# Optimization experiments

Hardware: AMD Instinct MI355X
Metric: run time of the kernel (lower is better)

Reference implementation:

```python
import jax, jax.numpy as jnp
import numpy as np

B, T = 32, 256
INPUT_DIM, TRAJ_TYPE_DIM = 10000, 32
HIDDEN, N_LAYERS, EMBED = 512, 2, 256
OUTPUT_DIM = 10000


def setup_inputs() -> dict:
    key = jax.random.key(0)
    ks = jax.random.split(key, 16)
    s = 0.05
    inp = {
        "locations": jax.random.randint(ks[0], (B, T), 0, INPUT_DIM),
        "times": jax.random.uniform(ks[1], (B, T, 1), dtype=jnp.float32),
        "labels": jax.random.randint(ks[2], (B,), 0, TRAJ_TYPE_DIM),
        "emb_table": jax.random.normal(ks[3], (INPUT_DIM, EMBED), jnp.float32) * s,
        "traj_emb": jax.random.normal(ks[4], (TRAJ_TYPE_DIM, HIDDEN * N_LAYERS), jnp.float32) * s,
        "w_ih0": jax.random.normal(ks[5], (3 * HIDDEN, EMBED + 1), jnp.float32) * s,
        "w_hh0": jax.random.normal(ks[6], (3 * HIDDEN, HIDDEN), jnp.float32) * s,
        "b_ih0": jax.random.normal(ks[7], (3 * HIDDEN,), jnp.float32) * s,
        "b_hh0": jax.random.normal(ks[8], (3 * HIDDEN,), jnp.float32) * s,
        "w_ih1": jax.random.normal(ks[9], (3 * HIDDEN, HIDDEN), jnp.float32) * s,
        "w_hh1": jax.random.normal(ks[10], (3 * HIDDEN, HIDDEN), jnp.float32) * s,
        "b_ih1": jax.random.normal(ks[11], (3 * HIDDEN,), jnp.float32) * s,
        "b_hh1": jax.random.normal(ks[12], (3 * HIDDEN,), jnp.float32) * s,
        "fc_w": jax.random.normal(ks[13], (OUTPUT_DIM + 1, HIDDEN), jnp.float32) * s,
        "fc_b": jax.random.normal(ks[14], (OUTPUT_DIM + 1,), jnp.float32) * s,
    }
    return inp


def _gru_layer(x_tbf, h0, w_ih, w_hh, b_ih, b_hh):
    # x_tbf: [T, B, F]; h0: [B, H]. Standard torch GRU cell math.
    x_gates = jnp.einsum("tbf,gf->tbg", x_tbf, w_ih) + b_ih  # [T,B,3H]

    def step(h, xg):
        hg = h @ w_hh.T + b_hh
        xr, xz, xn = jnp.split(xg, 3, axis=-1)
        hr, hz, hn = jnp.split(hg, 3, axis=-1)
        r = jax.nn.sigmoid(xr + hr)
        z = jax.nn.sigmoid(xz + hz)
        n = jnp.tanh(xn + r * hn)
        h_new = (1.0 - z) * n + z * h
        return h_new, h_new

    _, outs = jax.lax.scan(step, h0, x_gates)
    return outs  # [T, B, H]


def reference(locations, times, labels, emb_table, traj_emb,
              w_ih0, w_hh0, b_ih0, b_hh0, w_ih1, w_hh1, b_ih1, b_hh1,
              fc_w, fc_b):
    # init hidden: [B, L*H] -> flat view -> [L, B, H] (matches torch .view)
    h0 = traj_emb[labels].reshape(N_LAYERS, -1, HIDDEN)
    x = jnp.concatenate([emb_table[locations], times], axis=-1)  # [B,T,E+1]
    x = jnp.swapaxes(x, 0, 1)  # [T,B,E+1]
    x = _gru_layer(x, h0[0], w_ih0, w_hh0, b_ih0, b_hh0)
    x = _gru_layer(x, h0[1], w_ih1, w_hh1, b_ih1, b_hh1)
    out = jnp.swapaxes(x, 0, 1)  # [B,T,H]
    out = jax.nn.relu(out) @ fc_w.T + fc_b  # [B,T,OUT+1]
    location = jax.nn.log_softmax(out[:, :, :-1], axis=-1)
    time = jax.nn.sigmoid(out[:, :, -1])
    return (location, time)
```

## Files before the change

### kernel.cpp

```cpp
#include <hip/hip_runtime.h>

typedef unsigned short u16;
typedef __bf16 bf16x8 __attribute__((ext_vector_type(8)));
typedef float f32x4 __attribute__((ext_vector_type(4)));

#define DEVI __device__ __forceinline__

DEVI u16 f2b(float f) {
  union { float f; unsigned u; } c; c.f = f;
  unsigned r = c.u + 0x7FFFu + ((c.u >> 16) & 1u);
  return (u16)(r >> 16);
}

DEVI float sigm(float x) { return 1.f / (1.f + __expf(-x)); }
DEVI float tanhfast(float x) {
  x = fminf(fmaxf(x, -15.f), 15.f);
  float e = __expf(2.f * x);
  return (e - 1.f) / (e + 1.f);
}

DEVI void async16(const void* g, void* l) {
  __builtin_amdgcn_global_load_lds((const __attribute__((address_space(1))) void*)g,
                                   (__attribute__((address_space(3))) void*)l, 16, 0, 0);
}

DEVI f32x4 ld16cc(const u16* p) {
  f32x4 r;
  asm volatile("global_load_dwordx4 %0, %1, off sc0 sc1" : "=v"(r) : "v"(p) : "memory");
  return r;
}

__global__ __launch_bounds__(256) void k_castpad(const float* __restrict__ src, u16* __restrict__ dst,
                                                 int srows, int scols, int drows, int dcols) {
  size_t n = (size_t)drows * dcols;
  for (size_t i = blockIdx.x * 256 + threadIdx.x; i < n; i += (size_t)gridDim.x * 256) {
    int r = (int)(i / dcols), c = (int)(i % dcols);
    float v = (r < srows && c < scols) ? src[(size_t)r * scols + c] : 0.f;
    dst[i] = f2b(v);
  }
}

__global__ __launch_bounds__(256) void k_embed(const int* __restrict__ loc, const float* __restrict__ times,
                                               const float* __restrict__ emb, u16* __restrict__ x0) {
  int m = blockIdx.x * 4 + (threadIdx.x >> 6);
  int s = threadIdx.x & 63;
  int b = m & 31, t = m >> 5;
  int li = loc[b * 256 + t];
  const float4* er = (const float4*)(emb + (size_t)li * 256);
  u16* xr = x0 + (size_t)m * 288;
  float4 v = er[s];
  ushort4 u;
  u.x = f2b(v.x); u.y = f2b(v.y); u.z = f2b(v.z); u.w = f2b(v.w);
  *(ushort4*)(xr + s * 4) = u;
  if (s == 0) xr[256] = f2b(times[b * 256 + t]);
  else if (s <= 31) xr[256 + s] = 0;
}

__global__ __launch_bounds__(256) void k_hinit(const float* __restrict__ traj, const int* __restrict__ labels,
                                               u16* __restrict__ dst, int layer) {
  int idx = blockIdx.x * 256 + threadIdx.x;
  if (idx < 16384) {
    int fidx = layer * 16384 + idx;
    dst[idx] = f2b(traj[(size_t)labels[fidx >> 10] * 1024 + (fidx & 1023)]);
  }
}

template <int MODE>
__global__ __launch_bounds__(256) void k_gemm(const u16* __restrict__ A, const u16* __restrict__ Bw,
                                              const float* __restrict__ bias, float* __restrict__ C,
                                              int N, int K, float* __restrict__ tptr) {
  __shared__ __align__(16) u16 As[128 * 32];
  __shared__ __align__(16) u16 Bs[128 * 32];
  const int tid = threadIdx.x;
  const int lane = tid & 63, wid = tid >> 6;
  const int tn = blockIdx.x, tm = blockIdx.y;
  const int wm = wid >> 1, wn = wid & 1;

  f32x4 acc[4][4] = {};

  const int r0 = tid >> 2;
  const int cb0 = (tid * 16) & 63;

  for (int k0 = 0; k0 < K; k0 += 32) {
    __syncthreads();
#pragma unroll
    for (int p = 0; p < 2; ++p) {
      int row = r0 + p * 64;
      const u16* ga = A + (size_t)(tm * 128 + row) * K + k0 + (cb0 >> 1);
      async16(ga, (void*)(As + wid * 512 + p * 2048));
      const u16* gb = Bw + (size_t)(tn * 128 + row) * K + k0 + (cb0 >> 1);
      async16(gb, (void*)(Bs + wid * 512 + p * 2048));
    }
    asm volatile("s_waitcnt vmcnt(0)" ::: "memory");
    __syncthreads();
    bf16x8 af[4], bf[4];
#pragma unroll
    for (int i = 0; i < 4; ++i) {
      af[i] = *reinterpret_cast<const bf16x8*>(As + (wm * 64 + i * 16 + (lane & 15)) * 32 + ((lane >> 4) * 8));
      bf[i] = *reinterpret_cast<const bf16x8*>(Bs + (wn * 64 + i * 16 + (lane & 15)) * 32 + ((lane >> 4) * 8));
    }
#pragma unroll
    for (int i = 0; i < 4; ++i)
#pragma unroll
      for (int j = 0; j < 4; ++j)
        acc[i][j] = __builtin_amdgcn_mfma_f32_16x16x32_bf16(af[i], bf[j], acc[i][j], 0, 0, 0);
  }

  const int row0 = tm * 128 + wm * 64;
  const int col0 = tn * 128 + wn * 64;
#pragma unroll
  for (int i = 0; i < 4; ++i)
#pragma unroll
    for (int j = 0; j < 4; ++j)
#pragma unroll
      for (int r = 0; r < 4; ++r) {
        int row = row0 + i * 16 + ((lane >> 4) * 4) + r;
        int col = col0 + j * 16 + (lane & 15);
        float v = acc[i][j][r];
        if (MODE == 0) {
          C[(size_t)row * N + col] = v + bias[col];
        } else {
          int orow = ((row & 31) << 8) + (row >> 5);
          if (col < 10000) C[(size_t)orow * 10000 + col] = v + bias[col];
          else if (col == 10000) tptr[orow] = sigm(v + bias[col]);
        }
      }
}

#define NB 64

__global__ __launch_bounds__(512, 2) void k_scan2(
    const float* __restrict__ xg0,
    const u16* __restrict__ whh0, const float* __restrict__ bhh0,
    const u16* __restrict__ wih1, const float* __restrict__ bih1,
    const u16* __restrict__ whh1, const float* __restrict__ bhh1,
    const float* __restrict__ traj, const int* __restrict__ labels,
    u16* __restrict__ h0x, u16* __restrict__ h1x, float* __restrict__ x1x,
    u16* __restrict__ h1seq, int* __restrict__ flags)
{
  const int tid = threadIdx.x, bid = blockIdx.x;
  const int role = bid >> 5, blk = bid & 31;
  const int lane = tid & 63, wid = tid >> 6;
  __shared__ float smD[2][3][16][16];

  const int eb = tid >> 4, ejj = tid & 15;
  const int jg = (blk << 4) + ejj;

  const float* bhh = (role == 0) ? bhh0 : bhh1;
  int fidx = (role == 1 ? 16384 : 0) + eb * 512 + jg;
  float h_own = traj[(size_t)labels[fidx >> 10] * 1024 + (fidx & 1023)];
  const float bh_r = bhh[jg], bh_z = bhh[512 + jg], bh_n = bhh[1024 + jg];

  const int mt = (wid < 6) ? wid / 3 : 0, nt = (wid < 6) ? wid % 3 : 0;
  bf16x8 bfragH[16];
  bf16x8 bfragX[16];
  float bX = 0.f;
  if (wid < 6) {
    const u16* wh = (role == 0) ? whh0 : whh1;
    const u16* wrow = wh + (size_t)(nt * 512 + (blk << 4) + (lane & 15)) * 512 + ((lane >> 4) * 8);
#pragma unroll
    for (int ks = 0; ks < 16; ++ks)
      bfragH[ks] = *reinterpret_cast<const bf16x8*>(wrow + ks * 32);
    if (role == 0) {
      const u16* xrow = wih1 + (size_t)(nt * 512 + (blk << 4) + (lane & 15)) * 512 + ((lane >> 4) * 8);
#pragma unroll
      for (int ks = 0; ks < 16; ++ks)
        bfragX[ks] = *reinterpret_cast<const bf16x8*>(xrow + ks * 32);
      bX = bih1[nt * 512 + (blk << 4) + (lane & 15)];
    }
  }

  const u16* hsrc = (role == 0) ? h0x : h1x;
  u16* hdst = (role == 0) ? h0x : h1x;

  for (int s = 0; s < 258; ++s) {
    const int wp = s & 1, rp = (s + 1) & 1;
    if (role == 0) {
      if (s <= 256) {
        float gxr = 0.f, gxz = 0.f, gxn = 0.f;
        if (s < 256) {
          const float* q = xg0 + (size_t)s * 49152 + eb * 1536 + jg;
          gxr = q[0]; gxz = q[512]; gxn = q[1024];
        }
        if (wid < 6) {
          const u16* hs = hsrc + (rp << 14) + ((mt * 16 + (lane & 15)) << 9) + ((lane >> 4) * 8);
          f32x4 afr[16];
#pragma unroll
          for (int ks = 0; ks < 16; ++ks) afr[ks] = ld16cc(hs + ks * 32);
          asm volatile("s_waitcnt vmcnt(0)" ::: "memory");
          __builtin_amdgcn_sched_barrier(0);
          const int col = lane & 15, rb = (lane >> 4) << 2;
          if (s < 256) {
            f32x4 a0 = {0.f, 0.f, 0.f, 0.f}, a1 = {0.f, 0.f, 0.f, 0.f};
#pragma unroll
            for (int ks = 0; ks < 8; ++ks) {
              a0 = __builtin_amdgcn_mfma_f32_16x16x32_bf16(__builtin_bit_cast(bf16x8, afr[2 * ks]),     bfragH[2 * ks],     a0, 0, 0, 0);
              a1 = __builtin_amdgcn_mfma_f32_16x16x32_bf16(__builtin_bit_cast(bf16x8, afr[2 * ks + 1]), bfragH[2 * ks + 1], a1, 0, 0, 0);
            }
#pragma unroll
            for (int r = 0; r < 4; ++r) smD[mt][nt][rb + r][col] = a0[r] + a1[r];
          }
          if (s >= 1) {
            f32x4 c0 = {0.f, 0.f, 0.f, 0.f}, c1 = {0.f, 0.f, 0.f, 0.f};
#pragma unroll
            for (int ks = 0; ks < 8; ++ks) {
              c0 = __builtin_amdgcn_mfma_f32_16x16x32_bf16(__builtin_bit_cast(bf16x8, afr[2 * ks]),     bfragX[2 * ks],     c0, 0, 0, 0);
              c1 = __builtin_amdgcn_mfma_f32_16x16x32_bf16(__builtin_bit_cast(bf16x8, afr[2 * ks + 1]), bfragX[2 * ks + 1], c1, 0, 0, 0);
            }
            float* xp = x1x + wp * 49152;
#pragma unroll
            for (int r = 0; r < 4; ++r) {
              int ebr = mt * 16 + rb + r;
              __hip_atomic_store(xp + ((ebr * 3 + nt) << 9) + (blk << 4) + col,
                                 c0[r] + c1[r] + bX, __ATOMIC_RELAXED, __HIP_MEMORY_SCOPE_AGENT);
            }
          }
        }
        if (s < 256) {
          __syncthreads();
          float Dr = smD[eb >> 4][0][eb & 15][ejj] + bh_r;
          float Dz = smD[eb >> 4][1][eb & 15][ejj] + bh_z;
          float Dn = smD[eb >> 4][2][eb & 15][ejj] + bh_n;
          float r = sigm(gxr + Dr);
          float z = sigm(gxz + Dz);
          float n = tanhfast(gxn + r * Dn);
          h_own = (1.f - z) * n + z * h_own;
          unsigned hv = f2b(h_own);
          unsigned oth = __shfl_xor(hv, 1);
          if (!(ejj & 1))
            __hip_atomic_store((unsigned*)(hdst + (wp << 14)) + (((eb << 9) + jg) >> 1),
                               hv | (oth << 16), __ATOMIC_RELAXED, __HIP_MEMORY_SCOPE_AGENT);
        }
      }
    } else {
      if (s >= 2) {
        float* xp = x1x + rp * 49152 + ((eb * 3) << 9) + jg;
        float gxr = __hip_atomic_load(xp,        __ATOMIC_RELAXED, __HIP_MEMORY_SCOPE_AGENT);
        float gxz = __hip_atomic_load(xp + 512,  __ATOMIC_RELAXED, __HIP_MEMORY_SCOPE_AGENT);
        float gxn = __hip_atomic_load(xp + 1024, __ATOMIC_RELAXED, __HIP_MEMORY_SCOPE_AGENT);
        if (wid < 6) {
          const u16* hs = hsrc + (rp << 14) + ((mt * 16 + (lane & 15)) << 9) + ((lane >> 4) * 8);
          f32x4 afr[16];
#pragma unroll
          for (int ks = 0; ks < 16; ++ks) afr[ks] = ld16cc(hs + ks * 32);
          asm volatile("s_waitcnt vmcnt(0)" ::: "memory");
          __builtin_amdgcn_sched_barrier(0);
          f32x4 a0 = {0.f, 0.f, 0.f, 0.f}, a1 = {0.f, 0.f, 0.f, 0.f};
#pragma unroll
          for (int ks = 0; ks < 8; ++ks) {
            a0 = __builtin_amdgcn_mfma_f32_16x16x32_bf16(__builtin_bit_cast(bf16x8, afr[2 * ks]),     bfragH[2 * ks],     a0, 0, 0, 0);
            a1 = __builtin_amdgcn_mfma_f32_16x16x32_bf16(__builtin_bit_cast(bf16x8, afr[2 * ks + 1]), bfragH[2 * ks + 1], a1, 0, 0, 0);
          }
          const int col = lane & 15, rb = (lane >> 4) << 2;
#pragma unroll
          for (int r = 0; r < 4; ++r) smD[mt][nt][rb + r][col] = a0[r] + a1[r];
        }
        __syncthreads();
        float Dr = smD[eb >> 4][0][eb & 15][ejj] + bh_r;
        float Dz = smD[eb >> 4][1][eb & 15][ejj] + bh_z;
        float Dn = smD[eb >> 4][2][eb & 15][ejj] + bh_n;
        float r = sigm(gxr + Dr);
        float z = sigm(gxz + Dz);
        float n = tanhfast(gxn + r * Dn);
        h_own = (1.f - z) * n + z * h_own;
        unsigned hv = f2b(h_own);
        unsigned oth = __shfl_xor(hv, 1);
        if (!(ejj & 1))
          __hip_atomic_store((unsigned*)(hdst + (wp << 14)) + (((eb << 9) + jg) >> 1),
                             hv | (oth << 16), __ATOMIC_RELAXED, __HIP_MEMORY_SCOPE_AGENT);
        h1seq[((size_t)((s - 2) * 32 + eb) << 9) + jg] = f2b(fmaxf(h_own, 0.f));
      }
    }
    if (s < 257) {
      asm volatile("s_waitcnt vmcnt(0)" ::: "memory");
      __syncthreads();
      if (tid == 0) {
        __hip_atomic_fetch_add(flags + ((s * 8 + (bid & 7)) << 4), 1,
                               __ATOMIC_RELAXED, __HIP_MEMORY_SCOPE_AGENT);
        int* fb = flags + ((s * 8) << 4);
        int sum;
        do {
          sum = 0;
#pragma unroll
          for (int i = 0; i < 8; ++i)
            sum += __hip_atomic_load(fb + (i << 4), __ATOMIC_RELAXED, __HIP_MEMORY_SCOPE_AGENT);
        } while (sum < NB);
      }
      __syncthreads();
    }
  }
}

__global__ __launch_bounds__(256) void k_logsoftmax(float* __restrict__ out) {
  const int row = blockIdx.x, tid = threadIdx.x;
  float* p = out + (size_t)row * 10000;
  const int n_own = (tid < 16) ? 40 : 39;
  float v[40];
  float mx = -3.4e38f;
#pragma unroll
  for (int i = 0; i < 40; ++i)
    if (i < n_own) { v[i] = p[i * 256 + tid]; mx = fmaxf(mx, v[i]); }
  for (int o = 32; o; o >>= 1) mx = fmaxf(mx, __shfl_xor(mx, o));
  __shared__ float sm[4], ss[4];
  if ((tid & 63) == 0) sm[tid >> 6] = mx;
  __syncthreads();
  mx = fmaxf(fmaxf(sm[0], sm[1]), fmaxf(sm[2], sm[3]));
  float s = 0.f;
#pragma unroll
  for (int i = 0; i < 40; ++i)
    if (i < n_own) s += __expf(v[i] - mx);
  for (int o = 32; o; o >>= 1) s += __shfl_xor(s, o);
  if ((tid & 63) == 0) ss[tid >> 6] = s;
  __syncthreads();
  s = ss[0] + ss[1] + ss[2] + ss[3];
  float lse = mx + __logf(s);
#pragma unroll
  for (int i = 0; i < 40; ++i)
    if (i < n_own) p[i * 256 + tid] = v[i] - lse;
}

extern "C" void kernel_launch(void* const* d_in, const int* in_sizes, int n_in,
                              void* d_out, int out_size, void* d_ws, size_t ws_size,
                              hipStream_t stream) {
  (void)in_sizes; (void)n_in; (void)out_size;
  const int*   loc    = (const int*)  d_in[0];
  const float* times  = (const float*)d_in[1];
  const int*   labels = (const int*)  d_in[2];
  const float* emb    = (const float*)d_in[3];
  const float* traj   = (const float*)d_in[4];
  const float* w_ih0  = (const float*)d_in[5];
  const float* w_hh0  = (const float*)d_in[6];
  const float* b_ih0  = (const float*)d_in[7];
  const float* b_hh0  = (const float*)d_in[8];
  const float* w_ih1  = (const float*)d_in[9];
  const float* w_hh1  = (const float*)d_in[10];
  const float* b_ih1  = (const float*)d_in[11];
  const float* b_hh1  = (const float*)d_in[12];
  const float* fc_w   = (const float*)d_in[13];
  const float* fc_b   = (const float*)d_in[14];

  if (ws_size < 29800000) return;

  char* ws = (char*)d_ws;
  size_t off = 0;
  auto alloc = [&](size_t b) { size_t r = off; off += (b + 255) & ~(size_t)255; return r; };
  int*   flags = (int*)  (ws + alloc(258 * 8 * 16 * 4));
  u16*   h0x   = (u16*)  (ws + alloc(2 * 32 * 512 * 2));
  u16*   h1x   = (u16*)  (ws + alloc(2 * 32 * 512 * 2));
  float* x1x   = (float*)(ws + alloc(2 * 32 * 3 * 512 * 4));
  u16*   x0    = (u16*)  (ws + alloc((size_t)8192 * 288 * 2));
  u16*   wih0b = (u16*)  (ws + alloc((size_t)1536 * 288 * 2));
  u16*   whh0b = (u16*)  (ws + alloc((size_t)1536 * 512 * 2));
  u16*   wih1b = (u16*)  (ws + alloc((size_t)1536 * 512 * 2));
  u16*   whh1b = (u16*)  (ws + alloc((size_t)1536 * 512 * 2));
  u16*   fcwb  = (u16*)  (ws + alloc((size_t)10112 * 512 * 2));
  u16*   h1seq = (u16*)  (ws + alloc((size_t)8192 * 512 * 2));

  float* outp = (float*)d_out;
  float* xg0  = outp;
  float* tptr = outp + 81920000;

  hipMemsetAsync(flags, 0, 258 * 8 * 16 * 4, stream);
  k_castpad<<<1024, 256, 0, stream>>>(w_ih0, wih0b, 1536, 257, 1536, 288);
  k_castpad<<<1024, 256, 0, stream>>>(w_hh0, whh0b, 1536, 512, 1536, 512);
  k_castpad<<<1024, 256, 0, stream>>>(w_ih1, wih1b, 1536, 512, 1536, 512);
  k_castpad<<<1024, 256, 0, stream>>>(w_hh1, whh1b, 1536, 512, 1536, 512);
  k_castpad<<<1024, 256, 0, stream>>>(fc_w, fcwb, 10001, 512, 10112, 512);
  k_embed<<<2048, 256, 0, stream>>>(loc, times, emb, x0);
  k_gemm<0><<<dim3(12, 64), 256, 0, stream>>>(x0, wih0b, b_ih0, xg0, 1536, 288, nullptr);
  k_hinit<<<64, 256, 0, stream>>>(traj, labels, h0x + 16384, 0);
  k_hinit<<<64, 256, 0, stream>>>(traj, labels, h1x + 16384, 1);
  k_scan2<<<NB, 512, 0, stream>>>(xg0, whh0b, b_hh0, wih1b, b_ih1, whh1b, b_hh1,
                                  traj, labels, h0x, h1x, x1x, h1seq, flags);
  k_gemm<1><<<dim3(79, 64), 256, 0, stream>>>(h1seq, fcwb, fc_b, outp, 10112, 512, tptr);
  k_logsoftmax<<<8192, 256, 0, stream>>>(outp);
}
```

Before: 1.841 ms.

## Replace global grid barrier in GRU scan with per-step dataflow tags

The persistent two-layer GRU scan no longer uses a global all-block barrier every timestep. Each block now publishes a per-step tag (replicated 4x to spread polling) and waits only on the tags it depends on, so layer 0 can run up to several steps ahead of layer 1 through an 8-deep x1x ring buffer. The W_ih1 fragments move from registers into swizzled LDS to relieve register pressure. The risks are extra polling traffic, LDS reads on the critical path, and subtle ordering correctness under relaxed atomics.

Measured after the change: 1.735 ms. 1.06x faster.

```diff
diff --git a/kernel.cpp b/kernel.cpp
--- a/kernel.cpp
+++ b/kernel.cpp
@@ -65,6 +65,11 @@
   }
 }
 
+__global__ __launch_bounds__(128) void k_taginit(unsigned* __restrict__ tag0) {
+  int t = threadIdx.x;
+  tag0[(t >> 5) * 259 * 32 + (t & 31)] = 1u;
+}
+
 template <int MODE>
 __global__ __launch_bounds__(256) void k_gemm(const u16* __restrict__ A, const u16* __restrict__ Bw,
                                               const float* __restrict__ bias, float* __restrict__ C,
@@ -127,21 +132,21 @@
       }
 }
 
-#define NB 64
-
-__global__ __launch_bounds__(512, 2) void k_scan2(
-    const float* __restrict__ xg0,
-    const u16* __restrict__ whh0, const float* __restrict__ bhh0,
-    const u16* __restrict__ wih1, const float* __restrict__ bih1,
-    const u16* __restrict__ whh1, const float* __restrict__ bhh1,
-    const float* __restrict__ traj, const int* __restrict__ labels,
-    u16* __restrict__ h0x, u16* __restrict__ h1x, float* __restrict__ x1x,
-    u16* __restrict__ h1seq, int* __restrict__ flags)
+__global__ __launch_bounds__(512) __attribute__((amdgpu_waves_per_eu(2, 2)))
+void k_scan3(const float* __restrict__ xg0,
+             const u16* __restrict__ whh0, const float* __restrict__ bhh0,
+             const u16* __restrict__ wih1, const float* __restrict__ bih1,
+             const u16* __restrict__ whh1, const float* __restrict__ bhh1,
+             const float* __restrict__ traj, const int* __restrict__ labels,
+             u16* __restrict__ h0x, u16* __restrict__ h1x, float* __restrict__ x1x,
+             u16* __restrict__ h1seq, unsigned* __restrict__ tag0, unsigned* __restrict__ tag1)
 {
   const int tid = threadIdx.x, bid = blockIdx.x;
   const int role = bid >> 5, blk = bid & 31;
   const int lane = tid & 63, wid = tid >> 6;
+  const int rep = bid & 3;
   __shared__ float smD[2][3][16][16];
+  __shared__ __align__(16) u16 xlds[24576];
 
   const int eb = tid >> 4, ejj = tid & 15;
   const int jg = (blk << 4) + ejj;
@@ -153,7 +158,6 @@
 
   const int mt = (wid < 6) ? wid / 3 : 0, nt = (wid < 6) ? wid % 3 : 0;
   bf16x8 bfragH[16];
-  bf16x8 bfragX[16];
   float bX = 0.f;
   if (wid < 6) {
     const u16* wh = (role == 0) ? whh0 : whh1;
@@ -161,80 +165,103 @@
 #pragma unroll
     for (int ks = 0; ks < 16; ++ks)
       bfragH[ks] = *reinterpret_cast<const bf16x8*>(wrow + ks * 32);
-    if (role == 0) {
-      const u16* xrow = wih1 + (size_t)(nt * 512 + (blk << 4) + (lane & 15)) * 512 + ((lane >> 4) * 8);
-#pragma unroll
-      for (int ks = 0; ks < 16; ++ks)
-        bfragX[ks] = *reinterpret_cast<const bf16x8*>(xrow + ks * 32);
-      bX = bih1[nt * 512 + (blk << 4) + (lane & 15)];
-    }
-  }
+    if (role == 0) bX = bih1[nt * 512 + (blk << 4) + (lane & 15)];
+  }
+  if (role == 0) {
+    for (int c = tid; c < 3072; c += 512) {
+      int row = c >> 6, o16 = c & 63;
+      int grow = (row >> 4) * 512 + (blk << 4) + (row & 15);
+      const float4* src = (const float4*)(wih1 + (size_t)grow * 512 + o16 * 8);
+      int byte = (row << 10) + ((o16 * 16) ^ ((row & 7) << 4));
+      *(float4*)((char*)xlds + byte) = *src;
+    }
+  }
+  __syncthreads();
 
   const u16* hsrc = (role == 0) ? h0x : h1x;
   u16* hdst = (role == 0) ? h0x : h1x;
+  unsigned* mytag = (role == 0) ? tag0 : tag1;
 
   for (int s = 0; s < 258; ++s) {
-    const int wp = s & 1, rp = (s + 1) & 1;
+    if (role == 0 && s == 257) break;
+    const int rp = (s + 1) & 1, wp = s & 1;
+
     if (role == 0) {
-      if (s <= 256) {
-        float gxr = 0.f, gxz = 0.f, gxn = 0.f;
+      float gxr = 0.f, gxz = 0.f, gxn = 0.f;
+      if (s < 256) {
+        const float* q = xg0 + (size_t)s * 49152 + eb * 1536 + jg;
+        gxr = q[0]; gxz = q[512]; gxn = q[1024];
+      }
+      {
+        const unsigned* tp;
+        if (lane < 32)       tp = tag0 + ((size_t)(rep * 259 + s)) * 32 + lane;
+        else if (s >= 9)     tp = tag1 + ((size_t)(rep * 259 + (s - 6))) * 32 + (lane - 32);
+        else                 tp = tag0 + ((size_t)(rep * 259 + s)) * 32 + (lane - 32);
+        while (__ballot(__hip_atomic_load(tp, __ATOMIC_RELAXED, __HIP_MEMORY_SCOPE_AGENT) != 0u) != ~0ull) {}
+      }
+      if (wid < 6) {
+        const u16* hs = hsrc + (rp << 14) + ((mt * 16 + (lane & 15)) << 9) + ((lane >> 4) * 8);
+        f32x4 afr[16];
+#pragma unroll
+        for (int ks = 0; ks < 16; ++ks) afr[ks] = ld16cc(hs + ks * 32);
+        asm volatile("s_waitcnt vmcnt(0)" ::: "memory");
+        __builtin_amdgcn_sched_barrier(0);
+        const int col = lane & 15, rb = (lane >> 4) << 2;
         if (s < 256) {
-          const float* q = xg0 + (size_t)s * 49152 + eb * 1536 + jg;
-          gxr = q[0]; gxz = q[512]; gxn = q[1024];
-        }
-        if (wid < 6) {
-          const u16* hs = hsrc + (rp << 14) + ((mt * 16 + (lane & 15)) << 9) + ((lane >> 4) * 8);
-          f32x4 afr[16];
-#pragma unroll
-          for (int ks = 0; ks < 16; ++ks) afr[ks] = ld16cc(hs + ks * 32);
-          asm volatile("s_waitcnt vmcnt(0)" ::: "memory");
-          __builtin_amdgcn_sched_barrier(0);
-          const int col = lane & 15, rb = (lane >> 4) << 2;
-          if (s < 256) {
-            f32x4 a0 = {0.f, 0.f, 0.f, 0.f}, a1 = {0.f, 0.f, 0.f, 0.f};
-#pragma unroll
-            for (int ks = 0; ks < 8; ++ks) {
-              a0 = __builtin_amdgcn_mfma_f32_16x16x32_bf16(__builtin_bit_cast(bf16x8, afr[2 * ks]),     bfragH[2 * ks],     a0, 0, 0, 0);
-              a1 = __builtin_amdgcn_mfma_f32_16x16x32_bf16(__builtin_bit_cast(bf16x8, afr[2 * ks + 1]), bfragH[2 * ks + 1], a1, 0, 0, 0);
-            }
-#pragma unroll
-            for (int r = 0; r < 4; ++r) smD[mt][nt][rb + r][col] = a0[r] + a1[r];
+          f32x4 a0 = {0.f, 0.f, 0.f, 0.f}, a1 = {0.f, 0.f, 0.f, 0.f};
+#pragma unroll
+          for (int ks = 0; ks < 8; ++ks) {
+            a0 = __builtin_amdgcn_mfma_f32_16x16x32_bf16(__builtin_bit_cast(bf16x8, afr[2 * ks]),     bfragH[2 * ks],     a0, 0, 0, 0);
+            a1 = __builtin_amdgcn_mfma_f32_16x16x32_bf16(__builtin_bit_cast(bf16x8, afr[2 * ks + 1]), bfragH[2 * ks + 1], a1, 0, 0, 0);
           }
-          if (s >= 1) {
-            f32x4 c0 = {0.f, 0.f, 0.f, 0.f}, c1 = {0.f, 0.f, 0.f, 0.f};
-#pragma unroll
-            for (int ks = 0; ks < 8; ++ks) {
-              c0 = __builtin_amdgcn_mfma_f32_16x16x32_bf16(__builtin_bit_cast(bf16x8, afr[2 * ks]),     bfragX[2 * ks],     c0, 0, 0, 0);
-              c1 = __builtin_amdgcn_mfma_f32_16x16x32_bf16(__builtin_bit_cast(bf16x8, afr[2 * ks + 1]), bfragX[2 * ks + 1], c1, 0, 0, 0);
-            }
-            float* xp = x1x + wp * 49152;
-#pragma unroll
-            for (int r = 0; r < 4; ++r) {
-              int ebr = mt * 16 + rb + r;
-              __hip_atomic_store(xp + ((ebr * 3 + nt) << 9) + (blk << 4) + col,
-                                 c0[r] + c1[r] + bX, __ATOMIC_RELAXED, __HIP_MEMORY_SCOPE_AGENT);
-            }
+#pragma unroll
+          for (int r = 0; r < 4; ++r) smD[mt][nt][rb + r][col] = a0[r] + a1[r];
+        }
+        if (s >= 1) {
+          const char* xbase = (const char*)xlds + ((nt * 16 + col) << 10);
+          const int cb = (lane >> 4) << 4;
+          const int swz = ((col & 7) << 4);
+          f32x4 c0 = {0.f, 0.f, 0.f, 0.f}, c1 = {0.f, 0.f, 0.f, 0.f};
+#pragma unroll
+          for (int ks = 0; ks < 8; ++ks) {
+            bf16x8 x0 = *(const bf16x8*)(xbase + (((2 * ks) * 64 + cb) ^ swz));
+            bf16x8 x1 = *(const bf16x8*)(xbase + (((2 * ks + 1) * 64 + cb) ^ swz));
+            c0 = __builtin_amdgcn_mfma_f32_16x16x32_bf16(__builtin_bit_cast(bf16x8, afr[2 * ks]),     x0, c0, 0, 0, 0);
+            c1 = __builtin_amdgcn_mfma_f32_16x16x32_bf16(__builtin_bit_cast(bf16x8, afr[2 * ks + 1]), x1, c1, 0, 0, 0);
           }
-        }
-        if (s < 256) {
-          __syncthreads();
-          float Dr = smD[eb >> 4][0][eb & 15][ejj] + bh_r;
-          float Dz = smD[eb >> 4][1][eb & 15][ejj] + bh_z;
-          float Dn = smD[eb >> 4][2][eb & 15][ejj] + bh_n;
-          float r = sigm(gxr + Dr);
-          float z = sigm(gxz + Dz);
-          float n = tanhfast(gxn + r * Dn);
-          h_own = (1.f - z) * n + z * h_own;
-          unsigned hv = f2b(h_own);
-          unsigned oth = __shfl_xor(hv, 1);
-          if (!(ejj & 1))
-            __hip_atomic_store((unsigned*)(hdst + (wp << 14)) + (((eb << 9) + jg) >> 1),
-                               hv | (oth << 16), __ATOMIC_RELAXED, __HIP_MEMORY_SCOPE_AGENT);
-        }
+          float* xp = x1x + (size_t)((s - 1) & 7) * 49152;
+#pragma unroll
+          for (int r = 0; r < 4; ++r) {
+            int ebr = mt * 16 + rb + r;
+            __hip_atomic_store(xp + ((ebr * 3 + nt) << 9) + (blk << 4) + col,
+                               c0[r] + c1[r] + bX, __ATOMIC_RELAXED, __HIP_MEMORY_SCOPE_AGENT);
+          }
+        }
+      }
+      __syncthreads();
+      if (s < 256) {
+        float Dr = smD[eb >> 4][0][eb & 15][ejj] + bh_r;
+        float Dz = smD[eb >> 4][1][eb & 15][ejj] + bh_z;
+        float Dn = smD[eb >> 4][2][eb & 15][ejj] + bh_n;
+        float r = sigm(gxr + Dr);
+        float z = sigm(gxz + Dz);
+        float n = tanhfast(gxn + r * Dn);
+        h_own = (1.f - z) * n + z * h_own;
+        unsigned hv = f2b(h_own);
+        unsigned oth = __shfl_xor(hv, 1);
+        if (!(ejj & 1))
+          __hip_atomic_store((unsigned*)(hdst + (wp << 14)) + (((eb << 9) + jg) >> 1),
+                             hv | (oth << 16), __ATOMIC_RELAXED, __HIP_MEMORY_SCOPE_AGENT);
       }
     } else {
       if (s >= 2) {
-        float* xp = x1x + rp * 49152 + ((eb * 3) << 9) + jg;
+        {
+          const unsigned* tp = (lane < 32)
+              ? tag0 + ((size_t)(rep * 259 + s)) * 32 + lane
+              : tag1 + ((size_t)(rep * 259 + s)) * 32 + (lane - 32);
+          while (__ballot(__hip_atomic_load(tp, __ATOMIC_RELAXED, __HIP_MEMORY_SCOPE_AGENT) != 0u) != ~0ull) {}
+        }
+        float* xp = x1x + (size_t)((s - 2) & 7) * 49152 + ((eb * 3) << 9) + jg;
         float gxr = __hip_atomic_load(xp,        __ATOMIC_RELAXED, __HIP_MEMORY_SCOPE_AGENT);
         float gxz = __hip_atomic_load(xp + 512,  __ATOMIC_RELAXED, __HIP_MEMORY_SCOPE_AGENT);
         float gxn = __hip_atomic_load(xp + 1024, __ATOMIC_RELAXED, __HIP_MEMORY_SCOPE_AGENT);
@@ -271,22 +298,13 @@
         h1seq[((size_t)((s - 2) * 32 + eb) << 9) + jg] = f2b(fmaxf(h_own, 0.f));
       }
     }
-    if (s < 257) {
-      asm volatile("s_waitcnt vmcnt(0)" ::: "memory");
-      __syncthreads();
-      if (tid == 0) {
-        __hip_atomic_fetch_add(flags + ((s * 8 + (bid & 7)) << 4), 1,
-                               __ATOMIC_RELAXED, __HIP_MEMORY_SCOPE_AGENT);
-        int* fb = flags + ((s * 8) << 4);
-        int sum;
-        do {
-          sum = 0;
-#pragma unroll
-          for (int i = 0; i < 8; ++i)
-            sum += __hip_atomic_load(fb + (i << 4), __ATOMIC_RELAXED, __HIP_MEMORY_SCOPE_AGENT);
-        } while (sum < NB);
-      }
-      __syncthreads();
+    asm volatile("s_waitcnt vmcnt(0)" ::: "memory");
+    __syncthreads();
+    if (tid == 0 && s < 257) {
+#pragma unroll
+      for (int r = 0; r < 4; ++r)
+        __hip_atomic_store(mytag + ((size_t)(r * 259 + s + 1)) * 32 + blk, 1u,
+                           __ATOMIC_RELAXED, __HIP_MEMORY_SCOPE_AGENT);
     }
   }
 }
@@ -339,15 +357,16 @@
   const float* fc_w   = (const float*)d_in[13];
   const float* fc_b   = (const float*)d_in[14];
 
-  if (ws_size < 29800000) return;
+  if (ws_size < 32000000) return;
 
   char* ws = (char*)d_ws;
   size_t off = 0;
   auto alloc = [&](size_t b) { size_t r = off; off += (b + 255) & ~(size_t)255; return r; };
-  int*   flags = (int*)  (ws + alloc(258 * 8 * 16 * 4));
+  unsigned* tag0 = (unsigned*)(ws + alloc(4 * 259 * 32 * 4));
+  unsigned* tag1 = (unsigned*)(ws + alloc(4 * 259 * 32 * 4));
   u16*   h0x   = (u16*)  (ws + alloc(2 * 32 * 512 * 2));
   u16*   h1x   = (u16*)  (ws + alloc(2 * 32 * 512 * 2));
-  float* x1x   = (float*)(ws + alloc(2 * 32 * 3 * 512 * 4));
+  float* x1x   = (float*)(ws + alloc((size_t)8 * 32 * 3 * 512 * 4));
   u16*   x0    = (u16*)  (ws + alloc((size_t)8192 * 288 * 2));
   u16*   wih0b = (u16*)  (ws + alloc((size_t)1536 * 288 * 2));
   u16*   whh0b = (u16*)  (ws + alloc((size_t)1536 * 512 * 2));
@@ -360,7 +379,8 @@
   float* xg0  = outp;
   float* tptr = outp + 81920000;
 
-  hipMemsetAsync(flags, 0, 258 * 8 * 16 * 4, stream);
+  hipMemsetAsync(tag0, 0, 2 * 4 * 259 * 32 * 4, stream);
+  k_taginit<<<1, 128, 0, stream>>>(tag0);
   k_castpad<<<1024, 256, 0, stream>>>(w_ih0, wih0b, 1536, 257, 1536, 288);
   k_castpad<<<1024, 256, 0, stream>>>(w_hh0, whh0b, 1536, 512, 1536, 512);
   k_castpad<<<1024, 256, 0, stream>>>(w_ih1, wih1b, 1536, 512, 1536, 512);
@@ -370,8 +390,8 @@
   k_gemm<0><<<dim3(12, 64), 256, 0, stream>>>(x0, wih0b, b_ih0, xg0, 1536, 288, nullptr);
   k_hinit<<<64, 256, 0, stream>>>(traj, labels, h0x + 16384, 0);
   k_hinit<<<64, 256, 0, stream>>>(traj, labels, h1x + 16384, 1);
-  k_scan2<<<NB, 512, 0, stream>>>(xg0, whh0b, b_hh0, wih1b, b_ih1, whh1b, b_hh1,
-                                  traj, labels, h0x, h1x, x1x, h1seq, flags);
+  k_scan3<<<64, 512, 0, stream>>>(xg0, whh0b, b_hh0, wih1b, b_ih1, whh1b, b_hh1,
+                                  traj, labels, h0x, h1x, x1x, h1seq, tag0, tag1);
   k_gemm<1><<<dim3(79, 64), 256, 0, stream>>>(h1seq, fcwb, fc_b, outp, 10112, 512, tptr);
   k_logsoftmax<<<8192, 256, 0, stream>>>(outp);
 }
```
